# Kernel optimization log

Measured on AMD Instinct MI355X. Metric: run time of the kernel, lower is better.

The kernel has to match this reference:

```python
import jax, jax.numpy as jnp
import numpy as np

IN_FEATURES = 256
N_HEADS = 4
N_HIDDEN = 128  # out_features, concat=False
SLOPE = 0.1
NEG_INF = -9e15


def setup_inputs() -> dict:
    key = jax.random.key(0)
    k1, k2, k3, k4 = jax.random.split(key, 4)
    N = 8192
    h = jax.random.normal(k1, (N, IN_FEATURES), dtype=jnp.float32)
    adj_mat = jax.random.randint(k2, (N, N), 0, 2, dtype=jnp.int32)
    # xavier_normal with gain=1.414
    std_W = 1.414 * (2.0 / (IN_FEATURES + N_HIDDEN * N_HEADS)) ** 0.5
    W = jax.random.normal(k3, (IN_FEATURES, N_HIDDEN * N_HEADS), dtype=jnp.float32) * std_W
    std_a = 1.414 * (2.0 / (2 * N_HIDDEN + 1)) ** 0.5
    a = jax.random.normal(k4, (N_HEADS, 2 * N_HIDDEN, 1), dtype=jnp.float32) * std_a
    return {"h": h, "adj_mat": adj_mat, "W": W, "a": a}


def reference(h, adj_mat, W, a):
    N = h.shape[0]
    # linear projection -> [H, N, d]
    ht = (h @ W).reshape(N, N_HEADS, N_HIDDEN).transpose(1, 0, 2)
    # dropout is identity (eval / p effectively 0), then LeakyReLU
    ht = jnp.where(ht >= 0, ht, SLOPE * ht)
    # additive attention scores: src[h,i] + tgt[h,j]
    src = jnp.einsum('hnd,hd->hn', ht, a[:, :N_HIDDEN, 0])  # [H, N]
    tgt = jnp.einsum('hnd,hd->hn', ht, a[:, N_HIDDEN:, 0])  # [H, N]
    e = src[:, :, None] + tgt[:, None, :]                   # [H, N, N]
    e = jnp.where(adj_mat[None, :, :] > 0, e, NEG_INF)
    attn = jax.nn.softmax(e, axis=-1)
    # weighted sum and mean over heads (concat=False)
    out = jnp.einsum('hnm,hmd->hnd', attn, ht).mean(axis=0)  # [N, d]
    return out
```

## Files before the change

### kernel.cpp

```cpp
#include <hip/hip_runtime.h>


typedef unsigned short u16;
typedef unsigned int u32;
using bf16x8 = __attribute__((ext_vector_type(8))) short;
using f32x4  = __attribute__((ext_vector_type(4))) float;
using i32x4  = __attribute__((ext_vector_type(4))) int;

typedef const void __attribute__((address_space(1))) gas_void;
typedef void __attribute__((address_space(3))) las_void;
#define GLD16(g, l) __builtin_amdgcn_global_load_lds((gas_void*)(g), (las_void*)(l), 16, 0, 0)

__device__ __forceinline__ u16 f2bf(float f) {
  u32 u = __float_as_uint(f);
  return (u16)((u + 0x7FFFu + ((u >> 16) & 1u)) >> 16);
}
__device__ __forceinline__ float bf2f(u16 u) {
  return __uint_as_float(((u32)u) << 16);
}

__global__ void transpose_w(const float* __restrict__ W, float* __restrict__ Wt) {
  __shared__ float tile[32][33];
  int cb = blockIdx.x * 32, kb = blockIdx.y * 32;
  int tc = threadIdx.x & 31, tr = threadIdx.x >> 5;
  for (int p = 0; p < 32; p += 8)
    tile[tr + p][tc] = W[(size_t)(kb + tr + p) * 512 + cb + tc];
  __syncthreads();
  for (int p = 0; p < 32; p += 8)
    Wt[(size_t)(cb + tr + p) * 256 + kb + tc] = tile[tc][tr + p];
}

__global__ void ht_gemm(const float* __restrict__ h, const float* __restrict__ Wt,
                        u16* __restrict__ HT) {
  __shared__ __align__(16) u16 Abuf[128 * 40];
  __shared__ __align__(16) u16 Bbuf[128 * 40];
  int tid = threadIdx.x;
  int cb = blockIdx.x, rb = blockIdx.y;
  int r0 = rb * 128, c0 = cb * 128;
  int lane = tid & 63, wv = tid >> 6;
  int wr = wv >> 1, wc = wv & 1;
  int mrow = lane & 15, q = lane >> 4;
  int ch = tid & 7, m0 = tid >> 3;

  f32x4 acc[4][4];
#pragma unroll
  for (int i = 0; i < 4; i++)
#pragma unroll
    for (int j = 0; j < 4; j++) acc[i][j] = f32x4{0.f, 0.f, 0.f, 0.f};

  for (int kt = 0; kt < 256; kt += 32) {
    __syncthreads();
#pragma unroll
    for (int mp = 0; mp < 128; mp += 32) {
      int m = m0 + mp;
      float4 v = *(const float4*)(&h[(size_t)(r0 + m) * 256 + kt + ch * 4]);
      uint2 p;
      p.x = (u32)f2bf(v.x) | ((u32)f2bf(v.y) << 16);
      p.y = (u32)f2bf(v.z) | ((u32)f2bf(v.w) << 16);
      *(uint2*)(&Abuf[m * 40 + ch * 4]) = p;
      float4 u = *(const float4*)(&Wt[(size_t)(c0 + m) * 256 + kt + ch * 4]);
      uint2 r;
      r.x = (u32)f2bf(u.x) | ((u32)f2bf(u.y) << 16);
      r.y = (u32)f2bf(u.z) | ((u32)f2bf(u.w) << 16);
      *(uint2*)(&Bbuf[m * 40 + ch * 4]) = r;
    }
    __syncthreads();
    bf16x8 af[4], bfv[4];
#pragma unroll
    for (int i = 0; i < 4; i++)
      af[i] = *(const bf16x8*)(&Abuf[(wr * 64 + i * 16 + mrow) * 40 + q * 8]);
#pragma unroll
    for (int j = 0; j < 4; j++)
      bfv[j] = *(const bf16x8*)(&Bbuf[(wc * 64 + j * 16 + mrow) * 40 + q * 8]);
#pragma unroll
    for (int i = 0; i < 4; i++)
#pragma unroll
      for (int j = 0; j < 4; j++)
        acc[i][j] = __builtin_amdgcn_mfma_f32_16x16x32_bf16(af[i], bfv[j], acc[i][j], 0, 0, 0);
  }
#pragma unroll
  for (int i = 0; i < 4; i++)
#pragma unroll
    for (int j = 0; j < 4; j++)
#pragma unroll
      for (int r = 0; r < 4; r++) {
        int gi = r0 + wr * 64 + i * 16 + q * 4 + r;
        int gc = c0 + wc * 64 + j * 16 + mrow;
        float v = acc[i][j][r];
        v = v >= 0.f ? v : 0.1f * v;
        HT[(size_t)gi * 512 + gc] = f2bf(v);
      }
}

__global__ void build_yt(const u16* __restrict__ HT, const float* __restrict__ a,
                         u16* __restrict__ Yt) {
  __shared__ u16 sht[32][528];
  __shared__ float swv[32 * 4];
  __shared__ float sa[512];
  int t = threadIdx.x;
  int j0 = blockIdx.x * 32;
  for (int i = t; i < 512; i += 256) {
    int g = i >> 7, d = i & 127;
    sa[i] = a[g * 256 + 128 + d];
  }
#pragma unroll
  for (int p = 0; p < 8; ++p) {
    int el = t + 256 * p;
    int row = el >> 6, col8 = el & 63;
    *(uint4*)(&sht[row][col8 * 8]) = *(const uint4*)(&HT[(size_t)(j0 + row) * 512 + col8 * 8]);
  }
  __syncthreads();
  if (t < 128) {
    int jl = t >> 2, g = t & 3;
    float acc = 0.f;
#pragma unroll
    for (int d8 = 0; d8 < 16; ++d8) {
      bf16x8 v = *(const bf16x8*)(&sht[jl][g * 128 + d8 * 8]);
#pragma unroll
      for (int u = 0; u < 8; ++u)
        acc += bf2f((u16)v[u]) * sa[g * 128 + d8 * 8 + u];
    }
    swv[jl * 4 + g] = __expf(acc);
  }
  __syncthreads();
  int oj = (t & 3) * 8, oc = t >> 2;
  for (int pass = 0; pass < 9; ++pass) {
    int c = pass * 64 + oc;
    if (c >= 528) break;
    u32 pk[4] = {0u, 0u, 0u, 0u};
    if (c < 512) {
      int g = c >> 7;
#pragma unroll
      for (int u = 0; u < 4; ++u) {
        int j = oj + 2 * u;
        float v0 = bf2f(sht[j][c]) * swv[j * 4 + g];
        float v1 = bf2f(sht[j + 1][c]) * swv[(j + 1) * 4 + g];
        pk[u] = (u32)f2bf(v0) | ((u32)f2bf(v1) << 16);
      }
    } else if (c < 516) {
      int g = c - 512;
#pragma unroll
      for (int u = 0; u < 4; ++u) {
        int j = oj + 2 * u;
        float v0 = swv[j * 4 + g];
        float v1 = swv[(j + 1) * 4 + g];
        pk[u] = (u32)f2bf(v0) | ((u32)f2bf(v1) << 16);
      }
    }
    *(uint4*)(&Yt[(size_t)c * 8192 + j0 + oj]) = make_uint4(pk[0], pk[1], pk[2], pk[3]);
  }
}

__global__ __launch_bounds__(512) void adj_gemm(const int* __restrict__ adj,
                                                const u16* __restrict__ Yt,
                                                float* __restrict__ C,
                                                float* __restrict__ S) {
  __shared__ __align__(16) u16 Bbuf[3][512 * 32];
  __shared__ __align__(16) u16 Bden[3][16 * 32];
  __shared__ __align__(16) u16 Abuf[2][128 * 32];
  int tid = threadIdx.x;
  int rb = blockIdx.y, kh = blockIdx.x;
  int r0 = rb * 128, k0 = kh * 2048;
  int lane = tid & 63, wv = tid >> 6;
  int wr = wv >> 2, wc = wv & 3;
  int mrow = lane & 15, q = lane >> 4;
  int qs = q ^ ((mrow >> 1) & 3);
  int am = tid >> 2, aq = tid & 3;
  int asw = am * 32 + ((aq ^ ((am >> 1) & 3)) * 8);
  const int* abase = &adj[(size_t)(r0 + am) * 8192 + k0 + aq * 8];
  int brow = lane >> 2;
  int bq = (lane & 3) ^ ((lane >> 3) & 3);
  bool do_den = (wc == 0);

  f32x4 acc[4][8];
#pragma unroll
  for (int i = 0; i < 4; i++)
#pragma unroll
    for (int j = 0; j < 8; j++) acc[i][j] = f32x4{0.f, 0.f, 0.f, 0.f};
  f32x4 accD[4];
#pragma unroll
  for (int i = 0; i < 4; i++) accD[i] = f32x4{0.f, 0.f, 0.f, 0.f};

#define LOADA(V0, V1, TT)                                              \
  {                                                                    \
    const int* ap = abase + (size_t)(TT) * 32;                         \
    V0 = __builtin_nontemporal_load((const i32x4*)(ap));               \
    V1 = __builtin_nontemporal_load((const i32x4*)(ap + 4));           \
  }
#define PACKA(DST, V0, V1)                                             \
  {                                                                    \
    uint4 pk;                                                          \
    pk.x = 16256u * ((u32)V0[0] | ((u32)V0[1] << 16));                 \
    pk.y = 16256u * ((u32)V0[2] | ((u32)V0[3] << 16));                 \
    pk.z = 16256u * ((u32)V1[0] | ((u32)V1[1] << 16));                 \
    pk.w = 16256u * ((u32)V1[2] | ((u32)V1[3] << 16));                 \
    *(uint4*)((DST) + asw) = pk;                                       \
  }
#define STAGE_B(DB, DD, KT)                                            \
  {                                                                    \
    _Pragma("unroll") for (int p = 0; p < 4; ++p)                      \
        GLD16(&Yt[(size_t)(p * 128 + wv * 16 + brow) * 8192 + (KT) + bq * 8], \
              (DB) + (p * 128 + wv * 16) * 32);                        \
    if (wv == 0)                                                       \
      GLD16(&Yt[(size_t)(512 + brow) * 8192 + (KT) + bq * 8], (DD));   \
  }
#define WAIT_KEEP_ONE()                                                \
  {                                                                    \
    if (wv == 0) asm volatile("s_waitcnt vmcnt(5)" ::: "memory");      \
    else         asm volatile("s_waitcnt vmcnt(4)" ::: "memory");      \
  }

  {
    i32x4 a0, a1;
    LOADA(a0, a1, 0);
    __builtin_amdgcn_sched_barrier(0);
    STAGE_B(&Bbuf[0][0], &Bden[0][0], k0);
    STAGE_B(&Bbuf[1][0], &Bden[1][0], k0 + 32);
    PACKA(&Abuf[0][0], a0, a1);
    WAIT_KEEP_ONE();
    asm volatile("s_waitcnt lgkmcnt(0)" ::: "memory");
    __builtin_amdgcn_s_barrier();
  }

  u16 *bcur = &Bbuf[0][0], *bnxt = &Bbuf[1][0], *bnn = &Bbuf[2][0];
  u16 *dcur = &Bden[0][0], *dnxt = &Bden[1][0], *dnn = &Bden[2][0];

  for (int t = 0; t < 64; ++t) {
    i32x4 v0, v1;
    if (t < 63) {
      LOADA(v0, v1, t + 1);
      __builtin_amdgcn_sched_barrier(0);
    }
    if (t < 62) STAGE_B(bnn, dnn, k0 + (t + 2) * 32);
    bf16x8 af[4], bfv[8];
    const u16* Ab = &Abuf[t & 1][0];
#pragma unroll
    for (int i = 0; i < 4; i++)
      af[i] = *(const bf16x8*)(&Ab[(wr * 64 + i * 16 + mrow) * 32 + qs * 8]);
#pragma unroll
    for (int j = 0; j < 8; j++)
      bfv[j] = *(const bf16x8*)(&bcur[(wc * 128 + j * 16 + mrow) * 32 + qs * 8]);
    __builtin_amdgcn_s_setprio(1);
#pragma unroll
    for (int i = 0; i < 4; i++)
#pragma unroll
      for (int j = 0; j < 8; j++)
        acc[i][j] = __builtin_amdgcn_mfma_f32_16x16x32_bf16(af[i], bfv[j], acc[i][j], 0, 0, 0);
    if (do_den) {
      bf16x8 bd = *(const bf16x8*)(&dcur[mrow * 32 + qs * 8]);
#pragma unroll
      for (int i = 0; i < 4; i++)
        accD[i] = __builtin_amdgcn_mfma_f32_16x16x32_bf16(af[i], bd, accD[i], 0, 0, 0);
    }
    __builtin_amdgcn_s_setprio(0);
    if (t < 63) PACKA(&Abuf[(t + 1) & 1][0], v0, v1);
    if (t < 62) {
      WAIT_KEEP_ONE();
    } else if (t == 62) {
      asm volatile("s_waitcnt vmcnt(0)" ::: "memory");
    }
    if (t < 63) {
      asm volatile("s_waitcnt lgkmcnt(0)" ::: "memory");
      __builtin_amdgcn_s_barrier();
    }
    u16* tb = bcur; bcur = bnxt; bnxt = bnn; bnn = tb;
    u16* td = dcur; dcur = dnxt; dnxt = dnn; dnn = td;
  }
#undef LOADA
#undef PACKA
#undef STAGE_B
#undef WAIT_KEEP_ONE

  float* Ck = C + (size_t)kh * 8192 * 512;
#pragma unroll
  for (int i = 0; i < 4; i++)
#pragma unroll
    for (int j = 0; j < 8; j++)
#pragma unroll
      for (int r = 0; r < 4; r++) {
        int gi = r0 + wr * 64 + i * 16 + q * 4 + r;
        int gc = wc * 128 + j * 16 + mrow;
        Ck[(size_t)gi * 512 + gc] = acc[i][j][r];
      }
  if (do_den && mrow < 4) {
    float* Sk = S + (size_t)kh * 4 * 8192;
#pragma unroll
    for (int i = 0; i < 4; i++)
#pragma unroll
      for (int r = 0; r < 4; r++) {
        int gi = r0 + wr * 64 + i * 16 + q * 4 + r;
        Sk[(size_t)mrow * 8192 + gi] = accD[i][r];
      }
  }
}

__global__ void finalize_gat(const float* __restrict__ C, const float* __restrict__ S,
                             float* __restrict__ out) {
  int idx = blockIdx.x * 256 + threadIdx.x;
  int i = idx >> 7, d = idx & 127;
  float s = 0.f;
#pragma unroll
  for (int g = 0; g < 4; ++g) {
    float num = 0.f, den = 0.f;
#pragma unroll
    for (int kh = 0; kh < 4; ++kh) {
      num += C[(size_t)kh * 8192 * 512 + (size_t)i * 512 + g * 128 + d];
      den += S[(size_t)kh * 4 * 8192 + (size_t)g * 8192 + i];
    }
    s += num / den;
  }
  out[idx] = 0.25f * s;
}

extern "C" void kernel_launch(void* const* d_in, const int* in_sizes, int n_in,
                              void* d_out, int out_size, void* d_ws, size_t ws_size,
                              hipStream_t stream) {
  const float* h   = (const float*)d_in[0];
  const int*   adj = (const int*)d_in[1];
  const float* W   = (const float*)d_in[2];
  const float* a   = (const float*)d_in[3];
  float* out = (float*)d_out;
  char* ws = (char*)d_ws;
  float* Wt = (float*)(ws + 0);
  u16*   HT = (u16*)(ws + 524288);
  u16*   Yt = (u16*)(ws + 8912896);
  float* C  = (float*)(ws + 17563648);
  float* S  = (float*)(ws + 84672512);

  transpose_w<<<dim3(16, 8), 256, 0, stream>>>(W, Wt);
  ht_gemm<<<dim3(4, 64), 256, 0, stream>>>(h, Wt, HT);
  build_yt<<<dim3(256), 256, 0, stream>>>(HT, a, Yt);
  adj_gemm<<<dim3(4, 64), 512, 0, stream>>>(adj, Yt, C, S);
  finalize_gat<<<dim3(4096), 256, 0, stream>>>(C, S, out);
}
```

Measured before the change: 455.5 us.

## Store Yt in MFMA-fragment order and load B directly from global

The producer kernel now writes the bf16 Yt matrix in a tiled layout where each 32-wide k-tile of 16 columns forms a contiguous 512-element fragment matching the MFMA B operand lane order. adj_gemm drops the triple-buffered LDS staging of B (global_load_lds plus vmcnt waits) and reads B fragments straight from global or L2 into registers each k-step. This frees a large amount of LDS and removes the B stores into LDS and the reads back out. The cost is that B loads are no longer prefetched two tiles ahead, so global latency is exposed inside the loop. B data is also shared across the 4 wave-rows through cache rather than LDS, which raises L2 traffic.

```diff
diff --git a/kernel.cpp b/kernel.cpp
--- a/kernel.cpp
+++ b/kernel.cpp
@@ -6,10 +6,6 @@
 using bf16x8 = __attribute__((ext_vector_type(8))) short;
 using f32x4  = __attribute__((ext_vector_type(4))) float;
 using i32x4  = __attribute__((ext_vector_type(4))) int;
-
-typedef const void __attribute__((address_space(1))) gas_void;
-typedef void __attribute__((address_space(3))) las_void;
-#define GLD16(g, l) __builtin_amdgcn_global_load_lds((gas_void*)(g), (las_void*)(l), 16, 0, 0)
 
 __device__ __forceinline__ u16 f2bf(float f) {
   u32 u = __float_as_uint(f);
@@ -124,6 +120,7 @@
   }
   __syncthreads();
   int oj = (t & 3) * 8, oc = t >> 2;
+  size_t T = j0 >> 5;
   for (int pass = 0; pass < 9; ++pass) {
     int c = pass * 64 + oc;
     if (c >= 528) break;
@@ -147,7 +144,8 @@
         pk[u] = (u32)f2bf(v0) | ((u32)f2bf(v1) << 16);
       }
     }
-    *(uint4*)(&Yt[(size_t)c * 8192 + j0 + oj]) = make_uint4(pk[0], pk[1], pk[2], pk[3]);
+    size_t dst = ((size_t)(c >> 4) * 256 + T) * 512 + (size_t)(oj >> 3) * 128 + (c & 15) * 8;
+    *(uint4*)(&Yt[dst]) = make_uint4(pk[0], pk[1], pk[2], pk[3]);
   }
 }
 
@@ -155,8 +153,6 @@
                                                 const u16* __restrict__ Yt,
                                                 float* __restrict__ C,
                                                 float* __restrict__ S) {
-  __shared__ __align__(16) u16 Bbuf[3][512 * 32];
-  __shared__ __align__(16) u16 Bden[3][16 * 32];
   __shared__ __align__(16) u16 Abuf[2][128 * 32];
   int tid = threadIdx.x;
   int rb = blockIdx.y, kh = blockIdx.x;
@@ -168,9 +164,9 @@
   int am = tid >> 2, aq = tid & 3;
   int asw = am * 32 + ((aq ^ ((am >> 1) & 3)) * 8);
   const int* abase = &adj[(size_t)(r0 + am) * 8192 + k0 + aq * 8];
-  int brow = lane >> 2;
-  int bq = (lane & 3) ^ ((lane >> 3) & 3);
   bool do_den = (wc == 0);
+  const u16* ybase = Yt + ((size_t)(wc * 8) * 256 + (k0 >> 5)) * 512 + (size_t)lane * 8;
+  const u16* dbase = Yt + ((size_t)32 * 256 + (k0 >> 5)) * 512 + (size_t)lane * 8;
 
   f32x4 acc[4][8];
 #pragma unroll
@@ -196,80 +192,47 @@
     pk.w = 16256u * ((u32)V1[2] | ((u32)V1[3] << 16));                 \
     *(uint4*)((DST) + asw) = pk;                                       \
   }
-#define STAGE_B(DB, DD, KT)                                            \
-  {                                                                    \
-    _Pragma("unroll") for (int p = 0; p < 4; ++p)                      \
-        GLD16(&Yt[(size_t)(p * 128 + wv * 16 + brow) * 8192 + (KT) + bq * 8], \
-              (DB) + (p * 128 + wv * 16) * 32);                        \
-    if (wv == 0)                                                       \
-      GLD16(&Yt[(size_t)(512 + brow) * 8192 + (KT) + bq * 8], (DD));   \
-  }
-#define WAIT_KEEP_ONE()                                                \
-  {                                                                    \
-    if (wv == 0) asm volatile("s_waitcnt vmcnt(5)" ::: "memory");      \
-    else         asm volatile("s_waitcnt vmcnt(4)" ::: "memory");      \
-  }
 
   {
     i32x4 a0, a1;
     LOADA(a0, a1, 0);
-    __builtin_amdgcn_sched_barrier(0);
-    STAGE_B(&Bbuf[0][0], &Bden[0][0], k0);
-    STAGE_B(&Bbuf[1][0], &Bden[1][0], k0 + 32);
     PACKA(&Abuf[0][0], a0, a1);
-    WAIT_KEEP_ONE();
+  }
+  asm volatile("s_waitcnt lgkmcnt(0)" ::: "memory");
+  __builtin_amdgcn_s_barrier();
+
+  for (int t = 0; t < 64; ++t) {
+    bf16x8 bfv[8];
+#pragma unroll
+    for (int j = 0; j < 8; j++)
+      bfv[j] = *(const bf16x8*)(ybase + ((size_t)j * 256 + t) * 512);
+    bf16x8 bd;
+    if (do_den) bd = *(const bf16x8*)(dbase + (size_t)t * 512);
+    i32x4 v0, v1;
+    if (t < 63) LOADA(v0, v1, t + 1);
+    bf16x8 af[4];
+    const u16* Ab = &Abuf[t & 1][0];
+#pragma unroll
+    for (int i = 0; i < 4; i++)
+      af[i] = *(const bf16x8*)(&Ab[(wr * 64 + i * 16 + mrow) * 32 + qs * 8]);
+    __builtin_amdgcn_s_setprio(1);
+#pragma unroll
+    for (int j = 0; j < 8; j++)
+#pragma unroll
+      for (int i = 0; i < 4; i++)
+        acc[i][j] = __builtin_amdgcn_mfma_f32_16x16x32_bf16(af[i], bfv[j], acc[i][j], 0, 0, 0);
+    if (do_den) {
+#pragma unroll
+      for (int i = 0; i < 4; i++)
+        accD[i] = __builtin_amdgcn_mfma_f32_16x16x32_bf16(af[i], bd, accD[i], 0, 0, 0);
+    }
+    __builtin_amdgcn_s_setprio(0);
+    if (t < 63) PACKA(&Abuf[(t + 1) & 1][0], v0, v1);
     asm volatile("s_waitcnt lgkmcnt(0)" ::: "memory");
     __builtin_amdgcn_s_barrier();
   }
-
-  u16 *bcur = &Bbuf[0][0], *bnxt = &Bbuf[1][0], *bnn = &Bbuf[2][0];
-  u16 *dcur = &Bden[0][0], *dnxt = &Bden[1][0], *dnn = &Bden[2][0];
-
-  for (int t = 0; t < 64; ++t) {
-    i32x4 v0, v1;
-    if (t < 63) {
-      LOADA(v0, v1, t + 1);
-      __builtin_amdgcn_sched_barrier(0);
-    }
-    if (t < 62) STAGE_B(bnn, dnn, k0 + (t + 2) * 32);
-    bf16x8 af[4], bfv[8];
-    const u16* Ab = &Abuf[t & 1][0];
-#pragma unroll
-    for (int i = 0; i < 4; i++)
-      af[i] = *(const bf16x8*)(&Ab[(wr * 64 + i * 16 + mrow) * 32 + qs * 8]);
-#pragma unroll
-    for (int j = 0; j < 8; j++)
-      bfv[j] = *(const bf16x8*)(&bcur[(wc * 128 + j * 16 + mrow) * 32 + qs * 8]);
-    __builtin_amdgcn_s_setprio(1);
-#pragma unroll
-    for (int i = 0; i < 4; i++)
-#pragma unroll
-      for (int j = 0; j < 8; j++)
-        acc[i][j] = __builtin_amdgcn_mfma_f32_16x16x32_bf16(af[i], bfv[j], acc[i][j], 0, 0, 0);
-    if (do_den) {
-      bf16x8 bd = *(const bf16x8*)(&dcur[mrow * 32 + qs * 8]);
-#pragma unroll
-      for (int i = 0; i < 4; i++)
-        accD[i] = __builtin_amdgcn_mfma_f32_16x16x32_bf16(af[i], bd, accD[i], 0, 0, 0);
-    }
-    __builtin_amdgcn_s_setprio(0);
-    if (t < 63) PACKA(&Abuf[(t + 1) & 1][0], v0, v1);
-    if (t < 62) {
-      WAIT_KEEP_ONE();
-    } else if (t == 62) {
-      asm volatile("s_waitcnt vmcnt(0)" ::: "memory");
-    }
-    if (t < 63) {
-      asm volatile("s_waitcnt lgkmcnt(0)" ::: "memory");
-      __builtin_amdgcn_s_barrier();
-    }
-    u16* tb = bcur; bcur = bnxt; bnxt = bnn; bnn = tb;
-    u16* td = dcur; dcur = dnxt; dnxt = dnn; dnn = td;
-  }
 #undef LOADA
 #undef PACKA
-#undef STAGE_B
-#undef WAIT_KEEP_ONE
 
   float* Ck = C + (size_t)kh * 8192 * 512;
 #pragma unroll
```

New measurement: 467.6 us. 2.7% more time.

## Fuse attention-weight and Yt construction into the projection GEMM epilogue

Applied to the files above, without the earlier changes.

Removes the separate build_yt kernel and the intermediate HT buffer. The ht_gemm epilogue now applies LeakyReLU in registers and computes the per-row target score with lane shuffles plus a small LDS exchange between the two column waves. It then exponentiates and writes the scaled, transposed bf16 Yt directly. This is meant to save the HT write and re-read and one kernel launch. The risk is that Yt padding rows 516-527, which build_yt used to zero, are no longer written.

```diff
diff --git a/kernel.cpp b/kernel.cpp
--- a/kernel.cpp
+++ b/kernel.cpp
@@ -31,9 +31,10 @@
 }
 
 __global__ void ht_gemm(const float* __restrict__ h, const float* __restrict__ Wt,
-                        u16* __restrict__ HT) {
+                        const float* __restrict__ a, u16* __restrict__ Yt) {
   __shared__ __align__(16) u16 Abuf[128 * 40];
   __shared__ __align__(16) u16 Bbuf[128 * 40];
+  __shared__ float red[2][2][64];
   int tid = threadIdx.x;
   int cb = blockIdx.x, rb = blockIdx.y;
   int r0 = rb * 128, c0 = cb * 128;
@@ -78,76 +79,73 @@
       for (int j = 0; j < 4; j++)
         acc[i][j] = __builtin_amdgcn_mfma_f32_16x16x32_bf16(af[i], bfv[j], acc[i][j], 0, 0, 0);
   }
-#pragma unroll
-  for (int i = 0; i < 4; i++)
-#pragma unroll
-    for (int j = 0; j < 4; j++)
+
+#pragma unroll
+  for (int i = 0; i < 4; i++)
+#pragma unroll
+    for (int jj = 0; jj < 4; jj++)
 #pragma unroll
       for (int r = 0; r < 4; r++) {
-        int gi = r0 + wr * 64 + i * 16 + q * 4 + r;
-        int gc = c0 + wc * 64 + j * 16 + mrow;
-        float v = acc[i][j][r];
-        v = v >= 0.f ? v : 0.1f * v;
-        HT[(size_t)gi * 512 + gc] = f2bf(v);
+        float v = acc[i][jj][r];
+        acc[i][jj][r] = v >= 0.f ? v : 0.1f * v;
       }
-}
-
-__global__ void build_yt(const u16* __restrict__ HT, const float* __restrict__ a,
-                         u16* __restrict__ Yt) {
-  __shared__ u16 sht[32][528];
-  __shared__ float swv[32 * 4];
-  __shared__ float sa[512];
-  int t = threadIdx.x;
-  int j0 = blockIdx.x * 32;
-  for (int i = t; i < 512; i += 256) {
-    int g = i >> 7, d = i & 127;
-    sa[i] = a[g * 256 + 128 + d];
-  }
-#pragma unroll
-  for (int p = 0; p < 8; ++p) {
-    int el = t + 256 * p;
-    int row = el >> 6, col8 = el & 63;
-    *(uint4*)(&sht[row][col8 * 8]) = *(const uint4*)(&HT[(size_t)(j0 + row) * 512 + col8 * 8]);
-  }
+  float a2[4];
+#pragma unroll
+  for (int jj = 0; jj < 4; jj++)
+    a2[jj] = a[cb * 256 + 128 + wc * 64 + jj * 16 + mrow];
+  float part[4][4];
+#pragma unroll
+  for (int i = 0; i < 4; i++)
+#pragma unroll
+    for (int r = 0; r < 4; r++) {
+      float s = 0.f;
+#pragma unroll
+      for (int jj = 0; jj < 4; jj++) s += acc[i][jj][r] * a2[jj];
+      part[i][r] = s;
+    }
+#pragma unroll
+  for (int mask = 1; mask <= 8; mask <<= 1)
+#pragma unroll
+    for (int i = 0; i < 4; i++)
+#pragma unroll
+      for (int r = 0; r < 4; r++)
+        part[i][r] += __shfl_xor(part[i][r], mask);
+  if (mrow == 0)
+#pragma unroll
+    for (int i = 0; i < 4; i++)
+#pragma unroll
+      for (int r = 0; r < 4; r++)
+        red[wc][wr][i * 16 + q * 4 + r] = part[i][r];
   __syncthreads();
-  if (t < 128) {
-    int jl = t >> 2, g = t & 3;
-    float acc = 0.f;
-#pragma unroll
-    for (int d8 = 0; d8 < 16; ++d8) {
-      bf16x8 v = *(const bf16x8*)(&sht[jl][g * 128 + d8 * 8]);
-#pragma unroll
-      for (int u = 0; u < 8; ++u)
-        acc += bf2f((u16)v[u]) * sa[g * 128 + d8 * 8 + u];
-    }
-    swv[jl * 4 + g] = __expf(acc);
-  }
-  __syncthreads();
-  int oj = (t & 3) * 8, oc = t >> 2;
-  for (int pass = 0; pass < 9; ++pass) {
-    int c = pass * 64 + oc;
-    if (c >= 528) break;
-    u32 pk[4] = {0u, 0u, 0u, 0u};
-    if (c < 512) {
-      int g = c >> 7;
-#pragma unroll
-      for (int u = 0; u < 4; ++u) {
-        int j = oj + 2 * u;
-        float v0 = bf2f(sht[j][c]) * swv[j * 4 + g];
-        float v1 = bf2f(sht[j + 1][c]) * swv[(j + 1) * 4 + g];
-        pk[u] = (u32)f2bf(v0) | ((u32)f2bf(v1) << 16);
-      }
-    } else if (c < 516) {
-      int g = c - 512;
-#pragma unroll
-      for (int u = 0; u < 4; ++u) {
-        int j = oj + 2 * u;
-        float v0 = swv[j * 4 + g];
-        float v1 = swv[(j + 1) * 4 + g];
-        pk[u] = (u32)f2bf(v0) | ((u32)f2bf(v1) << 16);
-      }
-    }
-    *(uint4*)(&Yt[(size_t)c * 8192 + j0 + oj]) = make_uint4(pk[0], pk[1], pk[2], pk[3]);
+  float wexp[4][4];
+#pragma unroll
+  for (int i = 0; i < 4; i++)
+#pragma unroll
+    for (int r = 0; r < 4; r++)
+      wexp[i][r] = __expf(part[i][r] + red[wc ^ 1][wr][i * 16 + q * 4 + r]);
+
+#pragma unroll
+  for (int i = 0; i < 4; i++) {
+    int colb = r0 + wr * 64 + i * 16 + q * 4;
+#pragma unroll
+    for (int jj = 0; jj < 4; jj++) {
+      uint2 pk;
+      pk.x = (u32)f2bf(wexp[i][0] * acc[i][jj][0]) |
+             ((u32)f2bf(wexp[i][1] * acc[i][jj][1]) << 16);
+      pk.y = (u32)f2bf(wexp[i][2] * acc[i][jj][2]) |
+             ((u32)f2bf(wexp[i][3] * acc[i][jj][3]) << 16);
+      int row = cb * 128 + wc * 64 + jj * 16 + mrow;
+      *(uint2*)(&Yt[(size_t)row * 8192 + colb]) = pk;
+    }
+  }
+  if (wc == 0 && mrow == 0) {
+#pragma unroll
+    for (int i = 0; i < 4; i++) {
+      uint2 pk;
+      pk.x = (u32)f2bf(wexp[i][0]) | ((u32)f2bf(wexp[i][1]) << 16);
+      pk.y = (u32)f2bf(wexp[i][2]) | ((u32)f2bf(wexp[i][3]) << 16);
+      *(uint2*)(&Yt[(size_t)(512 + cb) * 8192 + r0 + wr * 64 + i * 16 + q * 4]) = pk;
+    }
   }
 }
 
@@ -322,14 +320,12 @@
   float* out = (float*)d_out;
   char* ws = (char*)d_ws;
   float* Wt = (float*)(ws + 0);
-  u16*   HT = (u16*)(ws + 524288);
   u16*   Yt = (u16*)(ws + 8912896);
   float* C  = (float*)(ws + 17563648);
   float* S  = (float*)(ws + 84672512);
 
   transpose_w<<<dim3(16, 8), 256, 0, stream>>>(W, Wt);
-  ht_gemm<<<dim3(4, 64), 256, 0, stream>>>(h, Wt, HT);
-  build_yt<<<dim3(256), 256, 0, stream>>>(HT, a, Yt);
+  ht_gemm<<<dim3(4, 64), 256, 0, stream>>>(h, Wt, a, Yt);
   adj_gemm<<<dim3(4, 64), 512, 0, stream>>>(adj, Yt, C, S);
   finalize_gat<<<dim3(4096), 256, 0, stream>>>(C, S, out);
 }
```

Result: no change. 452.3 us (-0.7%).
